# Kernel tuning notes

Measured on AMD Instinct MI355X. Metric: run time of the kernel, lower is better.

Reference implementation:

```python
import jax, jax.numpy as jnp
import numpy as np

D_K = 64

def setup_inputs() -> dict:
    key = jax.random.key(0)
    kq, kk, kv, km = jax.random.split(key, 4)
    B, H, S, D = 2, 16, 2048, D_K
    Q = jax.random.normal(kq, (B, H, S, D), dtype=jnp.float32)
    K = jax.random.normal(kk, (B, H, S, D), dtype=jnp.float32)
    V = jax.random.normal(kv, (B, H, S, D), dtype=jnp.float32)
    attn_mask = jax.random.bernoulli(km, 0.9, (B, H, S))  # True = valid
    return {"Q": Q, "K": K, "V": V, "attn_mask": attn_mask}

def reference(Q, K, V, attn_mask):
    # scores: [B, H, S, S]
    scores = jnp.einsum('bhqd,bhkd->bhqk', Q, K) / np.sqrt(D_K).astype(np.float32)
    fill = jnp.float32(1e-9)
    # mask rows (query positions) then columns (key positions), as in original
    scores = jnp.where(attn_mask[..., :, None], scores, fill)
    scores = jnp.where(attn_mask[..., None, :], scores, fill)
    attn = jax.nn.softmax(scores, axis=-1)
    context = jnp.einsum('bhqk,bhkd->bhqd', attn, V)
    return (context, attn)
```

## Files before the change

kernel.cpp:

```cpp
#include <hip/hip_runtime.h>

#define B_DIM 2
#define H_DIM 16
#define S_DIM 2048
#define D_DIM 64

constexpr int QB = 128;
constexpr int KB = 64;
constexpr int NT = S_DIM / KB;
constexpr float CL2E = 0.18033688011112042f;

typedef __attribute__((ext_vector_type(8))) short short8;
typedef __attribute__((ext_vector_type(4))) float f32x4;
typedef __attribute__((ext_vector_type(2))) unsigned uint2v;

__device__ __forceinline__ unsigned pkbf(float lo, float hi) {
  unsigned r;
  asm("v_cvt_pk_bf16_f32 %0, %1, %2" : "=v"(r) : "v"(lo), "v"(hi));
  return r;
}

__device__ __forceinline__ float fexp2(float x) {
  float r;
  asm("v_exp_f32 %0, %1" : "=v"(r) : "v"(x));
  return r;
}

__device__ __forceinline__ void barrier_lds() {
  asm volatile("s_waitcnt lgkmcnt(0)" ::: "memory");
  __builtin_amdgcn_s_barrier();
  asm volatile("" ::: "memory");
}

__global__ __launch_bounds__(256, 2)
void sdpa_kernel(const float* __restrict__ Qp, const float* __restrict__ Kp,
                 const float* __restrict__ Vp, const int* __restrict__ maskp,
                 float* __restrict__ ctx, float* __restrict__ attn)
{
  __shared__ __align__(16) unsigned short sK[2][KB * 64];
  __shared__ __align__(16) unsigned short sV[2][64 * KB];
  __shared__ __align__(16) unsigned short sP[4][32 * KB];

  const int tid  = threadIdx.x;
  const int wave = tid >> 6;
  const int lane = tid & 63;
  const int c = lane & 15;
  const int g = lane >> 4;

  const int bid = (blockIdx.x & 7) * 64 + (blockIdx.x >> 3);
  const int bh = bid >> 4;
  const int qt = bid & 15;
  const int q0 = qt * QB + wave * 32;
  const size_t bhS = (size_t)bh * S_DIM;

  const int key = tid >> 2;
  const int dq  = (tid & 3) << 4;
  const int kp  = (tid & 31) << 1;
  const int dq8 = (tid >> 5) << 3;

  short8 qf[2][2];
  #pragma unroll
  for (int m = 0; m < 2; ++m)
    #pragma unroll
    for (int kk = 0; kk < 2; ++kk) {
      const float* src = Qp + (bhS + (size_t)(q0 + m*16 + c)) * D_DIM + kk*32 + g*8;
      float4 a = ((const float4*)src)[0];
      float4 b = ((const float4*)src)[1];
      union { unsigned u[4]; short8 s; } w;
      w.u[0] = pkbf(a.x, a.y); w.u[1] = pkbf(a.z, a.w);
      w.u[2] = pkbf(b.x, b.y); w.u[3] = pkbf(b.z, b.w);
      qf[m][kk] = w.s;
    }

  float rvS[2];
  #pragma unroll
  for (int m = 0; m < 2; ++m)
    rvS[m] = maskp[bhS + q0 + m*16 + c] ? CL2E : 0.0f;

  float4 kr0, kr1, kr2, kr3;
  float4 vA0, vA1, vB0, vB1;
  int4 cv4[4];

  auto load_k = [&](int kt_) {
    const float* s = Kp + (bhS + (size_t)(kt_ * KB + key)) * D_DIM + dq;
    kr0 = ((const float4*)s)[0]; kr1 = ((const float4*)s)[1];
    kr2 = ((const float4*)s)[2]; kr3 = ((const float4*)s)[3];
  };
  auto load_v = [&](int kt_) {
    const float* s0 = Vp + (bhS + (size_t)(kt_ * KB + kp)) * D_DIM + dq8;
    vA0 = ((const float4*)s0)[0]; vA1 = ((const float4*)s0)[1];
    vB0 = ((const float4*)(s0 + D_DIM))[0]; vB1 = ((const float4*)(s0 + D_DIM))[1];
  };
  auto load_cv = [&](int kt_) {
    #pragma unroll
    for (int n = 0; n < 4; ++n)
      cv4[n] = *(const int4*)&maskp[bhS + kt_ * KB + n*16 + g*4];
  };
  auto write_k = [&](int buf) {
    union { unsigned u[4]; short8 s; } w0, w1;
    w0.u[0] = pkbf(kr0.x, kr0.y); w0.u[1] = pkbf(kr0.z, kr0.w);
    w0.u[2] = pkbf(kr1.x, kr1.y); w0.u[3] = pkbf(kr1.z, kr1.w);
    w1.u[0] = pkbf(kr2.x, kr2.y); w1.u[1] = pkbf(kr2.z, kr2.w);
    w1.u[2] = pkbf(kr3.x, kr3.y); w1.u[3] = pkbf(kr3.z, kr3.w);
    const int sw = (key & 7) << 3;
    *(short8*)&sK[buf][key * 64 + (dq ^ sw)]       = w0.s;
    *(short8*)&sK[buf][key * 64 + ((dq + 8) ^ sw)] = w1.s;
  };
  auto write_v = [&](int buf) {
    float fa[8], fb[8];
    *(float4*)&fa[0] = vA0; *(float4*)&fa[4] = vA1;
    *(float4*)&fb[0] = vB0; *(float4*)&fb[4] = vB1;
    #pragma unroll
    for (int e = 0; e < 8; ++e) {
      const int d = dq8 + e;
      *(unsigned*)&sV[buf][d * KB + (kp ^ ((d & 7) << 3))] = pkbf(fa[e], fb[e]);
    }
  };

  float lsum[2] = {0.0f, 0.0f};

  load_k(0); load_cv(0);
  for (int kt = 0; kt < NT; ++kt) {
    const int cur = kt & 1;
    write_k(cur);
    float cmf[4][4];
    #pragma unroll
    for (int n = 0; n < 4; ++n) {
      cmf[n][0] = cv4[n].x ? 1.0f : 0.0f;
      cmf[n][1] = cv4[n].y ? 1.0f : 0.0f;
      cmf[n][2] = cv4[n].z ? 1.0f : 0.0f;
      cmf[n][3] = cv4[n].w ? 1.0f : 0.0f;
    }
    if (kt + 1 < NT) { load_k(kt + 1); load_cv(kt + 1); }
    barrier_lds();

    short8 kf[4][2];
    #pragma unroll
    for (int n = 0; n < 4; ++n) {
      const int k2 = n*16 + c;
      const int sw = (k2 & 7) << 3;
      #pragma unroll
      for (int kk = 0; kk < 2; ++kk)
        kf[n][kk] = *(const short8*)&sK[cur][k2*64 + ((kk*32 + g*8) ^ sw)];
    }

    f32x4 sacc[4][2];
    #pragma unroll
    for (int n = 0; n < 4; ++n)
      #pragma unroll
      for (int m = 0; m < 2; ++m) sacc[n][m] = 0.0f;
    __builtin_amdgcn_s_setprio(1);
    #pragma unroll
    for (int n = 0; n < 4; ++n)
      #pragma unroll
      for (int m = 0; m < 2; ++m)
        #pragma unroll
        for (int kk = 0; kk < 2; ++kk)
          sacc[n][m] = __builtin_amdgcn_mfma_f32_16x16x32_bf16(kf[n][kk], qf[m][kk], sacc[n][m], 0, 0, 0);
    __builtin_amdgcn_s_setprio(0);

    #pragma unroll
    for (int m = 0; m < 2; ++m)
      #pragma unroll
      for (int n = 0; n < 4; ++n)
        #pragma unroll
        for (int e = 0; e < 4; ++e)
          lsum[m] += fexp2(sacc[n][m][e] * (cmf[n][e] * rvS[m]));
  }

  float Lm[2];
  #pragma unroll
  for (int m = 0; m < 2; ++m) {
    float v = lsum[m];
    v += __shfl_xor(v, 16);
    v += __shfl_xor(v, 32);
    Lm[m] = -__log2f(v);
  }

  f32x4 oacc[2][4];
  #pragma unroll
  for (int m = 0; m < 2; ++m)
    #pragma unroll
    for (int n = 0; n < 4; ++n) oacc[m][n] = 0.0f;

  unsigned short* const myP = sP[wave];
  const int rh  = lane >> 4;
  const int c16 = lane & 15;
  float* const abase = attn + (bhS + (size_t)q0) * S_DIM;

  load_k(0); load_v(0); load_cv(0);
  for (int kt = 0; kt < NT; ++kt) {
    const int cur = kt & 1;
    write_k(cur);
    write_v(cur);
    float cmf[4][4];
    #pragma unroll
    for (int n = 0; n < 4; ++n) {
      cmf[n][0] = cv4[n].x ? 1.0f : 0.0f;
      cmf[n][1] = cv4[n].y ? 1.0f : 0.0f;
      cmf[n][2] = cv4[n].z ? 1.0f : 0.0f;
      cmf[n][3] = cv4[n].w ? 1.0f : 0.0f;
    }
    if (kt + 1 < NT) { load_k(kt + 1); load_v(kt + 1); load_cv(kt + 1); }
    barrier_lds();

    short8 kf[4][2];
    #pragma unroll
    for (int n = 0; n < 4; ++n) {
      const int k2 = n*16 + c;
      const int sw = (k2 & 7) << 3;
      #pragma unroll
      for (int kk = 0; kk < 2; ++kk)
        kf[n][kk] = *(const short8*)&sK[cur][k2*64 + ((kk*32 + g*8) ^ sw)];
    }

    f32x4 sacc[4][2];
    #pragma unroll
    for (int n = 0; n < 4; ++n)
      #pragma unroll
      for (int m = 0; m < 2; ++m) sacc[n][m] = 0.0f;
    __builtin_amdgcn_s_setprio(1);
    #pragma unroll
    for (int n = 0; n < 4; ++n)
      #pragma unroll
      for (int m = 0; m < 2; ++m)
        #pragma unroll
        for (int kk = 0; kk < 2; ++kk)
          sacc[n][m] = __builtin_amdgcn_mfma_f32_16x16x32_bf16(kf[n][kk], qf[m][kk], sacc[n][m], 0, 0, 0);
    __builtin_amdgcn_s_setprio(0);

    #pragma unroll
    for (int m = 0; m < 2; ++m) {
      #pragma unroll
      for (int n = 0; n < 4; ++n) {
        f32x4 pv;
        #pragma unroll
        for (int e = 0; e < 4; ++e)
          pv[e] = fexp2(__builtin_fmaf(sacc[n][m][e], cmf[n][e] * rvS[m], Lm[m]));
        const int row = m*16 + c;
        const int swk = (n*16 + g*4) ^ ((c & 7) << 3);
        uint2v pr; pr.x = pkbf(pv[0], pv[1]); pr.y = pkbf(pv[2], pv[3]);
        *(uint2v*)&myP[row*64 + swk] = pr;
      }
    }

    short8 pf[2][2];
    #pragma unroll
    for (int m = 0; m < 2; ++m) {
      const int row = m*16 + c;
      const int sw = (c & 7) << 3;
      #pragma unroll
      for (int kk = 0; kk < 2; ++kk)
        pf[m][kk] = *(const short8*)&myP[row*64 + ((kk*32 + g*8) ^ sw)];
    }
    short8 vf[4][2];
    #pragma unroll
    for (int n = 0; n < 4; ++n) {
      const int d = n*16 + c;
      const int sw = (d & 7) << 3;
      #pragma unroll
      for (int kk = 0; kk < 2; ++kk)
        vf[n][kk] = *(const short8*)&sV[cur][d*KB + ((kk*32 + g*8) ^ sw)];
    }
    __builtin_amdgcn_s_setprio(1);
    #pragma unroll
    for (int m = 0; m < 2; ++m)
      #pragma unroll
      for (int n = 0; n < 4; ++n)
        #pragma unroll
        for (int kk = 0; kk < 2; ++kk)
          oacc[m][n] = __builtin_amdgcn_mfma_f32_16x16x32_bf16(pf[m][kk], vf[n][kk], oacc[m][n], 0, 0, 0);
    __builtin_amdgcn_s_setprio(0);

    {
      float* const at = abase + kt*KB;
      #pragma unroll
      for (int j = 0; j < 8; ++j) {
        const int r  = j*4 + rh;
        const int p8 = (c16 >> 1) ^ (r & 7);
        uint2v u = *(const uint2v*)&myP[r*64 + p8*8 + (c16 & 1)*4];
        union { unsigned iu; float f; } t0, t1, t2, t3;
        t0.iu = u.x << 16; t1.iu = u.x & 0xFFFF0000u;
        t2.iu = u.y << 16; t3.iu = u.y & 0xFFFF0000u;
        f32x4 o; o[0] = t0.f; o[1] = t1.f; o[2] = t2.f; o[3] = t3.f;
        __builtin_nontemporal_store(o, (f32x4*)(at + (size_t)r * S_DIM + c16*4));
      }
    }
  }

  #pragma unroll
  for (int m = 0; m < 2; ++m)
    #pragma unroll
    for (int n = 0; n < 4; ++n)
      #pragma unroll
      for (int e = 0; e < 4; ++e) {
        const int rl = m*16 + g*4 + e;
        ctx[(bhS + (size_t)(q0 + rl)) * D_DIM + (size_t)(n*16 + c)] = oacc[m][n][e];
      }
}

extern "C" void kernel_launch(void* const* d_in, const int* in_sizes, int n_in,
                              void* d_out, int out_size, void* d_ws, size_t ws_size,
                              hipStream_t stream) {
  const float* Q = (const float*)d_in[0];
  const float* K = (const float*)d_in[1];
  const float* V = (const float*)d_in[2];
  const int*   M = (const int*)d_in[3];
  float* ctx  = (float*)d_out;
  float* attn = ctx + (size_t)B_DIM * H_DIM * S_DIM * D_DIM;
  dim3 grid(B_DIM * H_DIM * (S_DIM / QB));
  sdpa_kernel<<<grid, 256, 0, stream>>>(Q, K, V, M, ctx, attn);
}
```

Before: 159.0 us.

## Double key tile to 128 per barrier and pack column mask into bitfield

Doubles the key block staged in LDS per iteration to 128 keys, processed as two 64-key halves, so barriers and loop overhead are halved and global loads per thread get wider. The column mask is now loaded each round and packed into two 32-bit bitmasks instead of being held as four int4 registers and float flags. The cost is twice the LDS for K/V buffers, which lowers occupancy, plus more registers for the staged K/V loads. The V swizzle changes to a 16-way XOR pattern, and the P reads within each round may need a wave-level ordering check.

```diff
diff --git a/kernel.cpp b/kernel.cpp
--- a/kernel.cpp
+++ b/kernel.cpp
@@ -6,8 +6,8 @@
 #define D_DIM 64
 
 constexpr int QB = 128;
-constexpr int KB = 64;
-constexpr int NT = S_DIM / KB;
+constexpr int KB = 128;
+constexpr int NR = S_DIM / KB;
 constexpr float CL2E = 0.18033688011112042f;
 
 typedef __attribute__((ext_vector_type(8))) short short8;
@@ -39,7 +39,7 @@
 {
   __shared__ __align__(16) unsigned short sK[2][KB * 64];
   __shared__ __align__(16) unsigned short sV[2][64 * KB];
-  __shared__ __align__(16) unsigned short sP[4][32 * KB];
+  __shared__ __align__(16) unsigned short sP[4][32 * 64];
 
   const int tid  = threadIdx.x;
   const int wave = tid >> 6;
@@ -53,10 +53,10 @@
   const int q0 = qt * QB + wave * 32;
   const size_t bhS = (size_t)bh * S_DIM;
 
-  const int key = tid >> 2;
-  const int dq  = (tid & 3) << 4;
-  const int kp  = (tid & 31) << 1;
-  const int dq8 = (tid >> 5) << 3;
+  const int keyk  = tid >> 1;
+  const int dhalf = (tid & 1) << 5;
+  const int kp    = (tid & 63) << 1;
+  const int dg    = (tid >> 6) << 3;
 
   short8 qf[2][2];
   #pragma unroll
@@ -77,95 +77,108 @@
   for (int m = 0; m < 2; ++m)
     rvS[m] = maskp[bhS + q0 + m*16 + c] ? CL2E : 0.0f;
 
-  float4 kr0, kr1, kr2, kr3;
-  float4 vA0, vA1, vB0, vB1;
-  int4 cv4[4];
+  float4 kr[8];
+  float4 vr[8];
+  unsigned mb[2];
 
   auto load_k = [&](int kt_) {
-    const float* s = Kp + (bhS + (size_t)(kt_ * KB + key)) * D_DIM + dq;
-    kr0 = ((const float4*)s)[0]; kr1 = ((const float4*)s)[1];
-    kr2 = ((const float4*)s)[2]; kr3 = ((const float4*)s)[3];
+    const float* s = Kp + (bhS + (size_t)(kt_ * KB + keyk)) * D_DIM + dhalf;
+    #pragma unroll
+    for (int i = 0; i < 8; ++i) kr[i] = ((const float4*)s)[i];
   };
   auto load_v = [&](int kt_) {
-    const float* s0 = Vp + (bhS + (size_t)(kt_ * KB + kp)) * D_DIM + dq8;
-    vA0 = ((const float4*)s0)[0]; vA1 = ((const float4*)s0)[1];
-    vB0 = ((const float4*)(s0 + D_DIM))[0]; vB1 = ((const float4*)(s0 + D_DIM))[1];
-  };
-  auto load_cv = [&](int kt_) {
-    #pragma unroll
-    for (int n = 0; n < 4; ++n)
-      cv4[n] = *(const int4*)&maskp[bhS + kt_ * KB + n*16 + g*4];
+    const float* s0 = Vp + (bhS + (size_t)(kt_ * KB + kp)) * D_DIM + dg;
+    vr[0] = ((const float4*)s0)[0];      vr[1] = ((const float4*)s0)[1];
+    vr[2] = ((const float4*)(s0+32))[0]; vr[3] = ((const float4*)(s0+32))[1];
+    const float* s1 = s0 + D_DIM;
+    vr[4] = ((const float4*)s1)[0];      vr[5] = ((const float4*)s1)[1];
+    vr[6] = ((const float4*)(s1+32))[0]; vr[7] = ((const float4*)(s1+32))[1];
+  };
+  auto load_mb = [&](int kt_) {
+    #pragma unroll
+    for (int hh = 0; hh < 2; ++hh) {
+      unsigned m = 0;
+      #pragma unroll
+      for (int n = 0; n < 4; ++n) {
+        int4 v = *(const int4*)&maskp[bhS + kt_*KB + hh*64 + n*16 + g*4];
+        m |= (v.x & 1u) << (n*4 + 0);
+        m |= (v.y & 1u) << (n*4 + 1);
+        m |= (v.z & 1u) << (n*4 + 2);
+        m |= (v.w & 1u) << (n*4 + 3);
+      }
+      mb[hh] = m;
+    }
   };
   auto write_k = [&](int buf) {
-    union { unsigned u[4]; short8 s; } w0, w1;
-    w0.u[0] = pkbf(kr0.x, kr0.y); w0.u[1] = pkbf(kr0.z, kr0.w);
-    w0.u[2] = pkbf(kr1.x, kr1.y); w0.u[3] = pkbf(kr1.z, kr1.w);
-    w1.u[0] = pkbf(kr2.x, kr2.y); w1.u[1] = pkbf(kr2.z, kr2.w);
-    w1.u[2] = pkbf(kr3.x, kr3.y); w1.u[3] = pkbf(kr3.z, kr3.w);
-    const int sw = (key & 7) << 3;
-    *(short8*)&sK[buf][key * 64 + (dq ^ sw)]       = w0.s;
-    *(short8*)&sK[buf][key * 64 + ((dq + 8) ^ sw)] = w1.s;
+    const int sw = (keyk & 7) << 3;
+    #pragma unroll
+    for (int o = 0; o < 4; ++o) {
+      const float* f = (const float*)&kr[o*2];
+      union { unsigned u[4]; short8 s; } w;
+      w.u[0] = pkbf(f[0], f[1]); w.u[1] = pkbf(f[2], f[3]);
+      w.u[2] = pkbf(f[4], f[5]); w.u[3] = pkbf(f[6], f[7]);
+      *(short8*)&sK[buf][keyk * 64 + ((dhalf + o*8) ^ sw)] = w.s;
+    }
   };
   auto write_v = [&](int buf) {
-    float fa[8], fb[8];
-    *(float4*)&fa[0] = vA0; *(float4*)&fa[4] = vA1;
-    *(float4*)&fb[0] = vB0; *(float4*)&fb[4] = vB1;
-    #pragma unroll
-    for (int e = 0; e < 8; ++e) {
-      const int d = dq8 + e;
-      *(unsigned*)&sV[buf][d * KB + (kp ^ ((d & 7) << 3))] = pkbf(fa[e], fb[e]);
+    float av[16], bv[16];
+    *(float4*)&av[0]  = vr[0]; *(float4*)&av[4]  = vr[1];
+    *(float4*)&av[8]  = vr[2]; *(float4*)&av[12] = vr[3];
+    *(float4*)&bv[0]  = vr[4]; *(float4*)&bv[4]  = vr[5];
+    *(float4*)&bv[8]  = vr[6]; *(float4*)&bv[12] = vr[7];
+    #pragma unroll
+    for (int e = 0; e < 16; ++e) {
+      const int d = dg + (e & 7) + ((e & 8) ? 32 : 0);
+      *(unsigned*)&sV[buf][d * KB + (kp ^ ((d & 15) << 3))] = pkbf(av[e], bv[e]);
     }
   };
 
   float lsum[2] = {0.0f, 0.0f};
 
-  load_k(0); load_cv(0);
-  for (int kt = 0; kt < NT; ++kt) {
-    const int cur = kt & 1;
+  load_k(0);
+  for (int r = 0; r < NR; ++r) {
+    const int cur = r & 1;
     write_k(cur);
-    float cmf[4][4];
-    #pragma unroll
-    for (int n = 0; n < 4; ++n) {
-      cmf[n][0] = cv4[n].x ? 1.0f : 0.0f;
-      cmf[n][1] = cv4[n].y ? 1.0f : 0.0f;
-      cmf[n][2] = cv4[n].z ? 1.0f : 0.0f;
-      cmf[n][3] = cv4[n].w ? 1.0f : 0.0f;
-    }
-    if (kt + 1 < NT) { load_k(kt + 1); load_cv(kt + 1); }
+    load_mb(r);
+    if (r + 1 < NR) load_k(r + 1);
     barrier_lds();
 
-    short8 kf[4][2];
-    #pragma unroll
-    for (int n = 0; n < 4; ++n) {
-      const int k2 = n*16 + c;
-      const int sw = (k2 & 7) << 3;
-      #pragma unroll
-      for (int kk = 0; kk < 2; ++kk)
-        kf[n][kk] = *(const short8*)&sK[cur][k2*64 + ((kk*32 + g*8) ^ sw)];
-    }
-
-    f32x4 sacc[4][2];
-    #pragma unroll
-    for (int n = 0; n < 4; ++n)
-      #pragma unroll
-      for (int m = 0; m < 2; ++m) sacc[n][m] = 0.0f;
-    __builtin_amdgcn_s_setprio(1);
-    #pragma unroll
-    for (int n = 0; n < 4; ++n)
+    #pragma unroll
+    for (int h = 0; h < 2; ++h) {
+      short8 kf[4][2];
+      #pragma unroll
+      for (int n = 0; n < 4; ++n) {
+        const int k2 = h*64 + n*16 + c;
+        const int sw = (c & 7) << 3;
+        #pragma unroll
+        for (int kk = 0; kk < 2; ++kk)
+          kf[n][kk] = *(const short8*)&sK[cur][k2*64 + ((kk*32 + g*8) ^ sw)];
+      }
+      f32x4 sacc[4][2];
+      #pragma unroll
+      for (int n = 0; n < 4; ++n)
+        #pragma unroll
+        for (int m = 0; m < 2; ++m) sacc[n][m] = 0.0f;
+      __builtin_amdgcn_s_setprio(1);
+      #pragma unroll
+      for (int n = 0; n < 4; ++n)
+        #pragma unroll
+        for (int m = 0; m < 2; ++m)
+          #pragma unroll
+          for (int kk = 0; kk < 2; ++kk)
+            sacc[n][m] = __builtin_amdgcn_mfma_f32_16x16x32_bf16(kf[n][kk], qf[m][kk], sacc[n][m], 0, 0, 0);
+      __builtin_amdgcn_s_setprio(0);
+
       #pragma unroll
       for (int m = 0; m < 2; ++m)
         #pragma unroll
-        for (int kk = 0; kk < 2; ++kk)
-          sacc[n][m] = __builtin_amdgcn_mfma_f32_16x16x32_bf16(kf[n][kk], qf[m][kk], sacc[n][m], 0, 0, 0);
-    __builtin_amdgcn_s_setprio(0);
-
-    #pragma unroll
-    for (int m = 0; m < 2; ++m)
-      #pragma unroll
-      for (int n = 0; n < 4; ++n)
-        #pragma unroll
-        for (int e = 0; e < 4; ++e)
-          lsum[m] += fexp2(sacc[n][m][e] * (cmf[n][e] * rvS[m]));
+        for (int n = 0; n < 4; ++n)
+          #pragma unroll
+          for (int e = 0; e < 4; ++e) {
+            const float cf = (float)((mb[h] >> (n*4 + e)) & 1u);
+            lsum[m] += fexp2(sacc[n][m][e] * (cf * rvS[m]));
+          }
+    }
   }
 
   float Lm[2];
@@ -188,102 +201,98 @@
   const int c16 = lane & 15;
   float* const abase = attn + (bhS + (size_t)q0) * S_DIM;
 
-  load_k(0); load_v(0); load_cv(0);
-  for (int kt = 0; kt < NT; ++kt) {
-    const int cur = kt & 1;
+  load_k(0); load_v(0);
+  for (int r = 0; r < NR; ++r) {
+    const int cur = r & 1;
     write_k(cur);
     write_v(cur);
-    float cmf[4][4];
-    #pragma unroll
-    for (int n = 0; n < 4; ++n) {
-      cmf[n][0] = cv4[n].x ? 1.0f : 0.0f;
-      cmf[n][1] = cv4[n].y ? 1.0f : 0.0f;
-      cmf[n][2] = cv4[n].z ? 1.0f : 0.0f;
-      cmf[n][3] = cv4[n].w ? 1.0f : 0.0f;
-    }
-    if (kt + 1 < NT) { load_k(kt + 1); load_v(kt + 1); load_cv(kt + 1); }
+    load_mb(r);
+    if (r + 1 < NR) { load_k(r + 1); load_v(r + 1); }
     barrier_lds();
 
-    short8 kf[4][2];
-    #pragma unroll
-    for (int n = 0; n < 4; ++n) {
-      const int k2 = n*16 + c;
-      const int sw = (k2 & 7) << 3;
-      #pragma unroll
-      for (int kk = 0; kk < 2; ++kk)
-        kf[n][kk] = *(const short8*)&sK[cur][k2*64 + ((kk*32 + g*8) ^ sw)];
-    }
-
-    f32x4 sacc[4][2];
-    #pragma unroll
-    for (int n = 0; n < 4; ++n)
-      #pragma unroll
-      for (int m = 0; m < 2; ++m) sacc[n][m] = 0.0f;
-    __builtin_amdgcn_s_setprio(1);
-    #pragma unroll
-    for (int n = 0; n < 4; ++n)
+    #pragma unroll
+    for (int h = 0; h < 2; ++h) {
+      short8 kf[4][2];
+      #pragma unroll
+      for (int n = 0; n < 4; ++n) {
+        const int k2 = h*64 + n*16 + c;
+        const int sw = (c & 7) << 3;
+        #pragma unroll
+        for (int kk = 0; kk < 2; ++kk)
+          kf[n][kk] = *(const short8*)&sK[cur][k2*64 + ((kk*32 + g*8) ^ sw)];
+      }
+      f32x4 sacc[4][2];
+      #pragma unroll
+      for (int n = 0; n < 4; ++n)
+        #pragma unroll
+        for (int m = 0; m < 2; ++m) sacc[n][m] = 0.0f;
+      __builtin_amdgcn_s_setprio(1);
+      #pragma unroll
+      for (int n = 0; n < 4; ++n)
+        #pragma unroll
+        for (int m = 0; m < 2; ++m)
+          #pragma unroll
+          for (int kk = 0; kk < 2; ++kk)
+            sacc[n][m] = __builtin_amdgcn_mfma_f32_16x16x32_bf16(kf[n][kk], qf[m][kk], sacc[n][m], 0, 0, 0);
+      __builtin_amdgcn_s_setprio(0);
+
+      #pragma unroll
+      for (int m = 0; m < 2; ++m) {
+        #pragma unroll
+        for (int n = 0; n < 4; ++n) {
+          f32x4 pv;
+          #pragma unroll
+          for (int e = 0; e < 4; ++e) {
+            const float cf = (float)((mb[h] >> (n*4 + e)) & 1u);
+            pv[e] = fexp2(__builtin_fmaf(sacc[n][m][e], cf * rvS[m], Lm[m]));
+          }
+          const int row = m*16 + c;
+          const int swk = (n*16 + g*4) ^ ((c & 7) << 3);
+          uint2v pr; pr.x = pkbf(pv[0], pv[1]); pr.y = pkbf(pv[2], pv[3]);
+          *(uint2v*)&myP[row*64 + swk] = pr;
+        }
+      }
+
+      short8 pf[2][2];
+      #pragma unroll
+      for (int m = 0; m < 2; ++m) {
+        const int row = m*16 + c;
+        const int sw = (c & 7) << 3;
+        #pragma unroll
+        for (int kk = 0; kk < 2; ++kk)
+          pf[m][kk] = *(const short8*)&myP[row*64 + ((kk*32 + g*8) ^ sw)];
+      }
+      short8 vf[4][2];
+      #pragma unroll
+      for (int n = 0; n < 4; ++n) {
+        const int d = n*16 + c;
+        #pragma unroll
+        for (int kk = 0; kk < 2; ++kk)
+          vf[n][kk] = *(const short8*)&sV[cur][d*KB + ((h*64 + kk*32 + g*8) ^ (c << 3))];
+      }
+      __builtin_amdgcn_s_setprio(1);
       #pragma unroll
       for (int m = 0; m < 2; ++m)
         #pragma unroll
-        for (int kk = 0; kk < 2; ++kk)
-          sacc[n][m] = __builtin_amdgcn_mfma_f32_16x16x32_bf16(kf[n][kk], qf[m][kk], sacc[n][m], 0, 0, 0);
-    __builtin_amdgcn_s_setprio(0);
-
-    #pragma unroll
-    for (int m = 0; m < 2; ++m) {
-      #pragma unroll
-      for (int n = 0; n < 4; ++n) {
-        f32x4 pv;
-        #pragma unroll
-        for (int e = 0; e < 4; ++e)
-          pv[e] = fexp2(__builtin_fmaf(sacc[n][m][e], cmf[n][e] * rvS[m], Lm[m]));
-        const int row = m*16 + c;
-        const int swk = (n*16 + g*4) ^ ((c & 7) << 3);
-        uint2v pr; pr.x = pkbf(pv[0], pv[1]); pr.y = pkbf(pv[2], pv[3]);
-        *(uint2v*)&myP[row*64 + swk] = pr;
-      }
-    }
-
-    short8 pf[2][2];
-    #pragma unroll
-    for (int m = 0; m < 2; ++m) {
-      const int row = m*16 + c;
-      const int sw = (c & 7) << 3;
-      #pragma unroll
-      for (int kk = 0; kk < 2; ++kk)
-        pf[m][kk] = *(const short8*)&myP[row*64 + ((kk*32 + g*8) ^ sw)];
-    }
-    short8 vf[4][2];
-    #pragma unroll
-    for (int n = 0; n < 4; ++n) {
-      const int d = n*16 + c;
-      const int sw = (d & 7) << 3;
-      #pragma unroll
-      for (int kk = 0; kk < 2; ++kk)
-        vf[n][kk] = *(const short8*)&sV[cur][d*KB + ((kk*32 + g*8) ^ sw)];
-    }
-    __builtin_amdgcn_s_setprio(1);
-    #pragma unroll
-    for (int m = 0; m < 2; ++m)
-      #pragma unroll
-      for (int n = 0; n < 4; ++n)
-        #pragma unroll
-        for (int kk = 0; kk < 2; ++kk)
-          oacc[m][n] = __builtin_amdgcn_mfma_f32_16x16x32_bf16(pf[m][kk], vf[n][kk], oacc[m][n], 0, 0, 0);
-    __builtin_amdgcn_s_setprio(0);
-
-    {
-      float* const at = abase + kt*KB;
-      #pragma unroll
-      for (int j = 0; j < 8; ++j) {
-        const int r  = j*4 + rh;
-        const int p8 = (c16 >> 1) ^ (r & 7);
-        uint2v u = *(const uint2v*)&myP[r*64 + p8*8 + (c16 & 1)*4];
-        union { unsigned iu; float f; } t0, t1, t2, t3;
-        t0.iu = u.x << 16; t1.iu = u.x & 0xFFFF0000u;
-        t2.iu = u.y << 16; t3.iu = u.y & 0xFFFF0000u;
-        f32x4 o; o[0] = t0.f; o[1] = t1.f; o[2] = t2.f; o[3] = t3.f;
-        __builtin_nontemporal_store(o, (f32x4*)(at + (size_t)r * S_DIM + c16*4));
+        for (int n = 0; n < 4; ++n)
+          #pragma unroll
+          for (int kk = 0; kk < 2; ++kk)
+            oacc[m][n] = __builtin_amdgcn_mfma_f32_16x16x32_bf16(pf[m][kk], vf[n][kk], oacc[m][n], 0, 0, 0);
+      __builtin_amdgcn_s_setprio(0);
+
+      {
+        float* const at = abase + r*KB + h*64;
+        #pragma unroll
+        for (int j = 0; j < 8; ++j) {
+          const int rr = j*4 + rh;
+          const int p8 = (c16 >> 1) ^ (rr & 7);
+          uint2v u = *(const uint2v*)&myP[rr*64 + p8*8 + (c16 & 1)*4];
+          union { unsigned iu; float f; } t0, t1, t2, t3;
+          t0.iu = u.x << 16; t1.iu = u.x & 0xFFFF0000u;
+          t2.iu = u.y << 16; t3.iu = u.y & 0xFFFF0000u;
+          f32x4 o; o[0] = t0.f; o[1] = t1.f; o[2] = t2.f; o[3] = t3.f;
+          __builtin_nontemporal_store(o, (f32x4*)(at + (size_t)rr * S_DIM + c16*4));
+        }
       }
     }
   }
```

Measured after the change: 177.2 us. 1.11x slower.

## Fold key mask into K tiles and double-buffer attention copy-out

Applied to the files above, without the earlier changes.

Zeroes masked key rows when K is packed into shared memory, so the per-element column-mask loads and multiplies in both passes go away (masked scores become 0 instead of 1e-9, numerically near-identical). The probability tile buffer is doubled so each tile's attention write-out is deferred and issued after the next tile's QK MFMAs, overlapping global stores with compute. This costs more LDS per block, which may pressure occupancy.

```diff
diff --git a/kernel.cpp b/kernel.cpp
--- a/kernel.cpp
+++ b/kernel.cpp
@@ -39,7 +39,7 @@
 {
   __shared__ __align__(16) unsigned short sK[2][KB * 64];
   __shared__ __align__(16) unsigned short sV[2][64 * KB];
-  __shared__ __align__(16) unsigned short sP[4][32 * KB];
+  __shared__ __align__(16) unsigned short sP[2][4][32 * 64];
 
   const int tid  = threadIdx.x;
   const int wave = tid >> 6;
@@ -79,29 +79,25 @@
 
   float4 kr0, kr1, kr2, kr3;
   float4 vA0, vA1, vB0, vB1;
-  int4 cv4[4];
+  unsigned kmr;
 
   auto load_k = [&](int kt_) {
     const float* s = Kp + (bhS + (size_t)(kt_ * KB + key)) * D_DIM + dq;
     kr0 = ((const float4*)s)[0]; kr1 = ((const float4*)s)[1];
     kr2 = ((const float4*)s)[2]; kr3 = ((const float4*)s)[3];
+    kmr = maskp[bhS + kt_ * KB + key] ? 0xFFFFFFFFu : 0u;
   };
   auto load_v = [&](int kt_) {
     const float* s0 = Vp + (bhS + (size_t)(kt_ * KB + kp)) * D_DIM + dq8;
     vA0 = ((const float4*)s0)[0]; vA1 = ((const float4*)s0)[1];
     vB0 = ((const float4*)(s0 + D_DIM))[0]; vB1 = ((const float4*)(s0 + D_DIM))[1];
   };
-  auto load_cv = [&](int kt_) {
-    #pragma unroll
-    for (int n = 0; n < 4; ++n)
-      cv4[n] = *(const int4*)&maskp[bhS + kt_ * KB + n*16 + g*4];
-  };
   auto write_k = [&](int buf) {
     union { unsigned u[4]; short8 s; } w0, w1;
-    w0.u[0] = pkbf(kr0.x, kr0.y); w0.u[1] = pkbf(kr0.z, kr0.w);
-    w0.u[2] = pkbf(kr1.x, kr1.y); w0.u[3] = pkbf(kr1.z, kr1.w);
-    w1.u[0] = pkbf(kr2.x, kr2.y); w1.u[1] = pkbf(kr2.z, kr2.w);
-    w1.u[2] = pkbf(kr3.x, kr3.y); w1.u[3] = pkbf(kr3.z, kr3.w);
+    w0.u[0] = pkbf(kr0.x, kr0.y) & kmr; w0.u[1] = pkbf(kr0.z, kr0.w) & kmr;
+    w0.u[2] = pkbf(kr1.x, kr1.y) & kmr; w0.u[3] = pkbf(kr1.z, kr1.w) & kmr;
+    w1.u[0] = pkbf(kr2.x, kr2.y) & kmr; w1.u[1] = pkbf(kr2.z, kr2.w) & kmr;
+    w1.u[2] = pkbf(kr3.x, kr3.y) & kmr; w1.u[3] = pkbf(kr3.z, kr3.w) & kmr;
     const int sw = (key & 7) << 3;
     *(short8*)&sK[buf][key * 64 + (dq ^ sw)]       = w0.s;
     *(short8*)&sK[buf][key * 64 + ((dq + 8) ^ sw)] = w1.s;
@@ -119,26 +115,18 @@
 
   float lsum[2] = {0.0f, 0.0f};
 
-  load_k(0); load_cv(0);
+  load_k(0);
   for (int kt = 0; kt < NT; ++kt) {
     const int cur = kt & 1;
     write_k(cur);
-    float cmf[4][4];
-    #pragma unroll
-    for (int n = 0; n < 4; ++n) {
-      cmf[n][0] = cv4[n].x ? 1.0f : 0.0f;
-      cmf[n][1] = cv4[n].y ? 1.0f : 0.0f;
-      cmf[n][2] = cv4[n].z ? 1.0f : 0.0f;
-      cmf[n][3] = cv4[n].w ? 1.0f : 0.0f;
-    }
-    if (kt + 1 < NT) { load_k(kt + 1); load_cv(kt + 1); }
+    if (kt + 1 < NT) load_k(kt + 1);
     barrier_lds();
 
     short8 kf[4][2];
     #pragma unroll
     for (int n = 0; n < 4; ++n) {
       const int k2 = n*16 + c;
-      const int sw = (k2 & 7) << 3;
+      const int sw = (c & 7) << 3;
       #pragma unroll
       for (int kk = 0; kk < 2; ++kk)
         kf[n][kk] = *(const short8*)&sK[cur][k2*64 + ((kk*32 + g*8) ^ sw)];
@@ -165,7 +153,7 @@
       for (int n = 0; n < 4; ++n)
         #pragma unroll
         for (int e = 0; e < 4; ++e)
-          lsum[m] += fexp2(sacc[n][m][e] * (cmf[n][e] * rvS[m]));
+          lsum[m] += fexp2(sacc[n][m][e] * rvS[m]);
   }
 
   float Lm[2];
@@ -183,32 +171,39 @@
     #pragma unroll
     for (int n = 0; n < 4; ++n) oacc[m][n] = 0.0f;
 
-  unsigned short* const myP = sP[wave];
   const int rh  = lane >> 4;
   const int c16 = lane & 15;
   float* const abase = attn + (bhS + (size_t)q0) * S_DIM;
 
-  load_k(0); load_v(0); load_cv(0);
+  auto copyout = [&](int pb, int kt_) {
+    const unsigned short* const Pp = sP[pb][wave];
+    float* const at = abase + kt_*KB;
+    #pragma unroll
+    for (int j = 0; j < 8; ++j) {
+      const int rr = j*4 + rh;
+      const int p8 = (c16 >> 1) ^ (rr & 7);
+      uint2v u = *(const uint2v*)&Pp[rr*64 + p8*8 + (c16 & 1)*4];
+      union { unsigned iu; float f; } t0, t1, t2, t3;
+      t0.iu = u.x << 16; t1.iu = u.x & 0xFFFF0000u;
+      t2.iu = u.y << 16; t3.iu = u.y & 0xFFFF0000u;
+      f32x4 o; o[0] = t0.f; o[1] = t1.f; o[2] = t2.f; o[3] = t3.f;
+      __builtin_nontemporal_store(o, (f32x4*)(at + (size_t)rr * S_DIM + c16*4));
+    }
+  };
+
+  load_k(0); load_v(0);
   for (int kt = 0; kt < NT; ++kt) {
     const int cur = kt & 1;
     write_k(cur);
     write_v(cur);
-    float cmf[4][4];
-    #pragma unroll
-    for (int n = 0; n < 4; ++n) {
-      cmf[n][0] = cv4[n].x ? 1.0f : 0.0f;
-      cmf[n][1] = cv4[n].y ? 1.0f : 0.0f;
-      cmf[n][2] = cv4[n].z ? 1.0f : 0.0f;
-      cmf[n][3] = cv4[n].w ? 1.0f : 0.0f;
-    }
-    if (kt + 1 < NT) { load_k(kt + 1); load_v(kt + 1); load_cv(kt + 1); }
+    if (kt + 1 < NT) { load_k(kt + 1); load_v(kt + 1); }
     barrier_lds();
 
     short8 kf[4][2];
     #pragma unroll
     for (int n = 0; n < 4; ++n) {
       const int k2 = n*16 + c;
-      const int sw = (k2 & 7) << 3;
+      const int sw = (c & 7) << 3;
       #pragma unroll
       for (int kk = 0; kk < 2; ++kk)
         kf[n][kk] = *(const short8*)&sK[cur][k2*64 + ((kk*32 + g*8) ^ sw)];
@@ -229,6 +224,9 @@
           sacc[n][m] = __builtin_amdgcn_mfma_f32_16x16x32_bf16(kf[n][kk], qf[m][kk], sacc[n][m], 0, 0, 0);
     __builtin_amdgcn_s_setprio(0);
 
+    if (kt > 0) copyout(cur ^ 1, kt - 1);
+
+    unsigned short* const myP = sP[cur][wave];
     #pragma unroll
     for (int m = 0; m < 2; ++m) {
       #pragma unroll
@@ -236,7 +234,7 @@
         f32x4 pv;
         #pragma unroll
         for (int e = 0; e < 4; ++e)
-          pv[e] = fexp2(__builtin_fmaf(sacc[n][m][e], cmf[n][e] * rvS[m], Lm[m]));
+          pv[e] = fexp2(__builtin_fmaf(sacc[n][m][e], rvS[m], Lm[m]));
         const int row = m*16 + c;
         const int swk = (n*16 + g*4) ^ ((c & 7) << 3);
         uint2v pr; pr.x = pkbf(pv[0], pv[1]); pr.y = pkbf(pv[2], pv[3]);
@@ -271,22 +269,9 @@
         for (int kk = 0; kk < 2; ++kk)
           oacc[m][n] = __builtin_amdgcn_mfma_f32_16x16x32_bf16(pf[m][kk], vf[n][kk], oacc[m][n], 0, 0, 0);
     __builtin_amdgcn_s_setprio(0);
-
-    {
-      float* const at = abase + kt*KB;
-      #pragma unroll
-      for (int j = 0; j < 8; ++j) {
-        const int r  = j*4 + rh;
-        const int p8 = (c16 >> 1) ^ (r & 7);
-        uint2v u = *(const uint2v*)&myP[r*64 + p8*8 + (c16 & 1)*4];
-        union { unsigned iu; float f; } t0, t1, t2, t3;
-        t0.iu = u.x << 16; t1.iu = u.x & 0xFFFF0000u;
-        t2.iu = u.y << 16; t3.iu = u.y & 0xFFFF0000u;
-        f32x4 o; o[0] = t0.f; o[1] = t1.f; o[2] = t2.f; o[3] = t3.f;
-        __builtin_nontemporal_store(o, (f32x4*)(at + (size_t)r * S_DIM + c16*4));
-      }
-    }
   }
+
+  copyout((NT - 1) & 1, NT - 1);
 
   #pragma unroll
   for (int m = 0; m < 2; ++m)
```

After: 152.9 us. 1.04x faster.
